# Performance work log

Measured on AMD Instinct MI355X. Metric: run time of the kernel, lower is better.

Reference implementation:

```python
import jax, jax.numpy as jnp
import numpy as np

N = 50000      # nodes
E = 800000     # edges (before self-loops)
IN_C = 128
HID = 32
HEADS = 4
OUT_C = 64
NEG_SLOPE = 0.2


def setup_inputs() -> dict:
    key = jax.random.key(0)
    ks = jax.random.split(key, 10)
    x = jax.random.normal(ks[0], (N, IN_C), dtype=jnp.float32)
    edge_index = jax.random.randint(ks[1], (2, E), 0, N, dtype=jnp.int32)
    # layer 1 params (GATConv(in_c, hid_c, heads=4), concat=True)
    W1 = jax.random.normal(ks[2], (IN_C, HEADS * HID), dtype=jnp.float32) / np.sqrt(IN_C)
    a_src1 = jax.random.normal(ks[3], (HEADS, HID), dtype=jnp.float32) / np.sqrt(HID)
    a_dst1 = jax.random.normal(ks[4], (HEADS, HID), dtype=jnp.float32) / np.sqrt(HID)
    b1 = jnp.zeros((HEADS * HID,), dtype=jnp.float32)
    # layer 2 params (GATConv(hid_c*heads, out_c, heads=1))
    W2 = jax.random.normal(ks[5], (HEADS * HID, OUT_C), dtype=jnp.float32) / np.sqrt(HEADS * HID)
    a_src2 = jax.random.normal(ks[6], (1, OUT_C), dtype=jnp.float32) / np.sqrt(OUT_C)
    a_dst2 = jax.random.normal(ks[7], (1, OUT_C), dtype=jnp.float32) / np.sqrt(OUT_C)
    b2 = jnp.zeros((OUT_C,), dtype=jnp.float32)
    return {"x": x, "edge_index": edge_index, "W1": W1, "a_src1": a_src1,
            "a_dst1": a_dst1, "b1": b1, "W2": W2, "a_src2": a_src2,
            "a_dst2": a_dst2, "b2": b2}


def _gat_layer(x, src, dst, self_mask, W, a_s, a_d, b, n):
    """One PyG-style GATConv: concat heads, leaky_relu(0.2), scatter-softmax over dst."""
    H, F = a_s.shape
    h = (x @ W).reshape(n, H, F)                       # [N, H, F]
    al_s = jnp.einsum('nhf,hf->nh', h, a_s)            # [N, H]
    al_d = jnp.einsum('nhf,hf->nh', h, a_d)
    e = al_s[src] + al_d[dst]                          # [E', H]
    e = jnp.where(e >= 0, e, NEG_SLOPE * e)            # leaky relu
    # emulate remove_self_loops on original edges (appended loops not masked)
    e = jnp.where(self_mask[:, None], -1e30, e)
    m = jax.ops.segment_max(e, dst, num_segments=n)    # per-dst max for stability
    p = jnp.exp(e - m[dst])
    p = jnp.where(self_mask[:, None], 0.0, p)
    denom = jax.ops.segment_sum(p, dst, num_segments=n) + 1e-16
    alpha = p / denom[dst]                             # [E', H]
    out = jax.ops.segment_sum(alpha[:, :, None] * h[src], dst, num_segments=n)
    return out.reshape(n, H * F) + b


def reference(x, edge_index, W1, a_src1, a_dst1, b1, W2, a_src2, a_dst2, b2):
    n = x.shape[0]
    src, dst = edge_index[0], edge_index[1]
    loops = jnp.arange(n, dtype=edge_index.dtype)
    src_a = jnp.concatenate([src, loops])
    dst_a = jnp.concatenate([dst, loops])
    # mask pre-existing self-loops (PyG removes then re-adds self loops)
    self_mask = jnp.concatenate([src == dst, jnp.zeros((n,), dtype=bool)])
    h = _gat_layer(x, src_a, dst_a, self_mask, W1, a_src1, a_dst1, b1, n)
    h = jax.nn.relu(h)
    return _gat_layer(h, src_a, dst_a, self_mask, W2, a_src2, a_dst2, b2, n)
```

## Files before the change

kernel.cpp:

```cpp
#include <hip/hip_runtime.h>

typedef unsigned short u16;
typedef unsigned int u32;
typedef __attribute__((ext_vector_type(8))) short bf16x8;
typedef __attribute__((ext_vector_type(4))) float f32x4;
typedef __attribute__((ext_vector_type(2))) float f32x2;

__device__ __forceinline__ float bf(u16 u){ return __uint_as_float(((u32)u) << 16); }
__device__ __forceinline__ float bf_lo(u32 u){ return __uint_as_float(u << 16); }
__device__ __forceinline__ float bf_hi(u32 u){ return __uint_as_float(u & 0xFFFF0000u); }
__device__ __forceinline__ u16 to_bf16(float f){
    u32 x = __float_as_uint(f);
    u32 r = (x + 0x7FFFu + ((x >> 16) & 1u)) >> 16;
    return (u16)r;
}
__device__ __forceinline__ float leaky(float v){ return (v >= 0.f) ? v : 0.2f * v; }
__device__ __forceinline__ float eexp(float v){
    return __expf(fminf(leaky(v), 80.f));
}
__device__ __forceinline__ f32x2 unpk2(u32 u){
    return (f32x2){bf_lo(u), bf_hi(u)};
}
__device__ __forceinline__ float ldany(const void* p, int i, int fl){
    return fl ? bf(((const u16*)p)[i]) : ((const float*)p)[i];
}
__device__ __forceinline__ u16 ldany_bf(const void* p, int i, int fl){
    return fl ? ((const u16*)p)[i] : to_bf16(((const float*)p)[i]);
}

constexpr int NS = 256;

struct HistCvtArgs {
    const int* dst; const int* src; int E; int chE; u16* cnt; int NBIN;
    const void* xin; u16* Xb; int nx;
    const void* W1; const void* W2; u16* W1t; u16* W2t;
    const void* vin[6]; float* vout[6];
    int* flag;
};
__global__ __launch_bounds__(256) void hist_cvt(HistCvtArgs a){
    int b = blockIdx.x;
    if (b < NS){
        __shared__ u32 hist[128];
        if (threadIdx.x < 128) hist[threadIdx.x] = 0;
        __syncthreads();
        int s0 = b * a.chE, s1 = min(a.E, s0 + a.chE);
        for (int i = s0 + threadIdx.x; i < s1; i += 256){
            int d = a.dst[i];
            if (a.src[i] != d) atomicAdd(&hist[d >> 9], 1);
        }
        __syncthreads();
        if (threadIdx.x < a.NBIN)
            a.cnt[threadIdx.x * NS + b] = (u16)hist[threadIdx.x];
        return;
    }
    __shared__ int sflag;
    const u16* x16 = (const u16*)a.xin;
    if (threadIdx.x < 64){
        int ok = 1;
        for (int i = threadIdx.x; i < 256; i += 64){
            u16 v = x16[i];
            int e = (v >> 7) & 0xFF;
            if (!((e >= 100 && e <= 140) || (v & 0x7FFFu) == 0)) ok = 0;
        }
        unsigned long long bl = __ballot(ok);
        if (threadIdx.x == 0) sflag = (__popcll(bl) >= 62) ? 1 : 0;
    }
    __syncthreads();
    int fl = sflag;
    int ci = (b - NS) * 256 + threadIdx.x;
    if (ci == 0) *a.flag = fl;
    if (ci < a.nx){ a.Xb[ci] = ldany_bf(a.xin, ci, fl); return; }
    ci -= a.nx;
    if (ci < 128 * 128){
        int n = ci >> 7, k = ci & 127;
        a.W1t[ci] = ldany_bf(a.W1, k * 128 + n, fl);
        return;
    }
    ci -= 128 * 128;
    if (ci < 64 * 128){
        int n = ci >> 7, k = ci & 127;
        a.W2t[ci] = ldany_bf(a.W2, k * 64 + n, fl);
        return;
    }
    ci -= 64 * 128;
    const int vsz[6] = {128, 128, 128, 64, 64, 64};
    #pragma unroll
    for (int s = 0; s < 6; s++){
        if (ci < vsz[s]){ a.vout[s][ci] = ldany(a.vin[s], ci, fl); return; }
        ci -= vsz[s];
    }
}

struct BucketGemmArgs {
    const int* dst; const int* src; int E; int chE; const u16* cnt; int NBIN;
    u32* Sbin;
    u32* bucket;
    const u16* Xb; const u16* W1t; u16* HB;
    const float* a_s; const float* a_d; float* al_s; float* al_d;
    int N;
};
__global__ __launch_bounds__(256) void bucket_gemm(BucketGemmArgs a){
    int b = blockIdx.x;
    if (b < NS){
        __shared__ u32 cur[128];
        __shared__ u32 Tl[129];
        int t = threadIdx.x;
        if (t < a.NBIN){
            const u16* row = a.cnt + (size_t)t * NS;
            u32 cb = 0, tot = 0;
            for (int sx = 0; sx < NS; sx++){
                u32 v = row[sx];
                tot += v;
                cb += (sx < b) ? v : 0u;
            }
            Tl[t + 1] = tot;
            cur[t] = cb;
        }
        __syncthreads();
        if (t == 0){
            u32 run = 0;
            Tl[0] = 0;
            for (int g = 1; g <= a.NBIN; g++){ run += Tl[g]; Tl[g] = run; }
        }
        __syncthreads();
        if (t < a.NBIN) cur[t] += Tl[t];
        if (b == 0 && t <= a.NBIN) a.Sbin[t] = Tl[t];
        __syncthreads();
        int s0 = b * a.chE, s1 = min(a.E, s0 + a.chE);
        for (int i = s0 + t; i < s1; i += 256){
            int d = a.dst[i];
            int s = a.src[i];
            if (s != d){
                u32 pos = atomicAdd(&cur[d >> 9], 1);
                a.bucket[pos] = ((u32)d << 16) | (u32)s;
            }
        }
        return;
    }
    int gb = b - NS;
    int lane = threadIdx.x & 63;
    int w = threadIdx.x >> 6;
    int row0 = gb * 64 + w * 16;
    int m = lane & 15, quad = lane >> 4;
    int arow = row0 + m;
    if (arow >= a.N) arow = a.N - 1;
    f32x4 acc[8];
    #pragma unroll
    for (int j = 0; j < 8; j++) acc[j] = (f32x4){0.f, 0.f, 0.f, 0.f};
    const u16* ap = a.Xb + (size_t)arow * 128 + quad * 8;
    const u16* bp = a.W1t + (size_t)m * 128 + quad * 8;
    #pragma unroll
    for (int kc = 0; kc < 4; kc++){
        bf16x8 av = *(const bf16x8*)(ap + kc * 32);
        #pragma unroll
        for (int nb = 0; nb < 8; nb++){
            bf16x8 bv = *(const bf16x8*)(bp + nb * 16 * 128 + kc * 32);
            acc[nb] = __builtin_amdgcn_mfma_f32_16x16x32_bf16(av, bv, acc[nb], 0, 0, 0);
        }
    }
    #pragma unroll
    for (int nb = 0; nb < 8; nb++){
        #pragma unroll
        for (int r = 0; r < 4; r++){
            int grow = row0 + quad * 4 + r;
            if (grow < a.N) a.HB[(size_t)grow * 128 + nb * 16 + m] = to_bf16(acc[nb][r]);
        }
    }
    float asr[8], adr[8];
    #pragma unroll
    for (int nb = 0; nb < 8; nb++){ asr[nb] = a.a_s[nb * 16 + m]; adr[nb] = a.a_d[nb * 16 + m]; }
    #pragma unroll
    for (int r = 0; r < 4; r++){
        int grow = row0 + quad * 4 + r;
        #pragma unroll
        for (int h = 0; h < 4; h++){
            float ps = acc[2 * h][r] * asr[2 * h] + acc[2 * h + 1][r] * asr[2 * h + 1];
            float pd = acc[2 * h][r] * adr[2 * h] + acc[2 * h + 1][r] * adr[2 * h + 1];
            #pragma unroll
            for (int d = 1; d < 16; d <<= 1){
                ps += __shfl_xor(ps, d);
                pd += __shfl_xor(pd, d);
            }
            if (m == h && grow < a.N){
                a.al_s[grow * 4 + h] = ps;
                a.al_d[grow * 4 + h] = pd;
            }
        }
    }
}

__global__ __launch_bounds__(256) void bin_csr(const u32* __restrict__ Sbin,
                                               const u32* __restrict__ bucket,
                                               int* __restrict__ off,
                                               u16* __restrict__ csr,
                                               int N, int NBIN){
    __shared__ u32 degL[512];
    __shared__ u32 curL[512];
    __shared__ int wsum[4];
    int b = blockIdx.x, t = threadIdx.x;
    int lo = b << 9;
    u32 base = Sbin[b];
    u32 end  = Sbin[b + 1];
    degL[t] = 0; degL[t + 256] = 0;
    __syncthreads();
    for (u32 i = base + t; i < end; i += 256){
        u32 pr = bucket[i];
        atomicAdd(&degL[(pr >> 16) - lo], 1);
    }
    __syncthreads();
    u32 d0 = degL[2 * t], d1 = degL[2 * t + 1];
    int p = (int)(d0 + d1);
    int v = p;
    #pragma unroll
    for (int d = 1; d < 64; d <<= 1){
        int o = __shfl_up(v, d);
        if ((t & 63) >= d) v += o;
    }
    if ((t & 63) == 63) wsum[t >> 6] = v;
    __syncthreads();
    int woff = 0;
    for (int wv = 0; wv < (t >> 6); wv++) woff += wsum[wv];
    int eb = woff + v - p;
    curL[2 * t] = eb;
    curL[2 * t + 1] = eb + d0;
    int n0 = lo + 2 * t, n1 = lo + 2 * t + 1;
    if (n0 < N) off[n0] = (int)(base + eb);
    if (n1 < N) off[n1] = (int)(base + eb + d0);
    if (b == NBIN - 1 && t == 255) off[N] = (int)end;
    __syncthreads();
    for (u32 i = base + t; i < end; i += 256){
        u32 pr = bucket[i];
        u32 pos = base + atomicAdd(&curL[(pr >> 16) - lo], 1);
        csr[pos] = (u16)(pr & 0xFFFF);
    }
}

__global__ __launch_bounds__(256) void gemm2_logits(const u16* __restrict__ Xb,
                                                    const u16* __restrict__ Wt,
                                                    u16* __restrict__ HB,
                                                    const float* __restrict__ a_s,
                                                    const float* __restrict__ a_d,
                                                    float* __restrict__ al_s,
                                                    float* __restrict__ al_d, int N){
    int lane = threadIdx.x & 63;
    int w = threadIdx.x >> 6;
    int row0 = blockIdx.x * 64 + w * 16;
    int m = lane & 15, quad = lane >> 4;
    int arow = row0 + m;
    if (arow >= N) arow = N - 1;
    f32x4 acc[4];
    #pragma unroll
    for (int j = 0; j < 4; j++) acc[j] = (f32x4){0.f, 0.f, 0.f, 0.f};
    const u16* ap = Xb + (size_t)arow * 128 + quad * 8;
    const u16* bp = Wt + (size_t)m * 128 + quad * 8;
    #pragma unroll
    for (int kc = 0; kc < 4; kc++){
        bf16x8 av = *(const bf16x8*)(ap + kc * 32);
        #pragma unroll
        for (int nb = 0; nb < 4; nb++){
            bf16x8 bv = *(const bf16x8*)(bp + nb * 16 * 128 + kc * 32);
            acc[nb] = __builtin_amdgcn_mfma_f32_16x16x32_bf16(av, bv, acc[nb], 0, 0, 0);
        }
    }
    #pragma unroll
    for (int nb = 0; nb < 4; nb++){
        #pragma unroll
        for (int r = 0; r < 4; r++){
            int grow = row0 + quad * 4 + r;
            if (grow < N) HB[(size_t)grow * 64 + nb * 16 + m] = to_bf16(acc[nb][r]);
        }
    }
    float asr[4], adr[4];
    #pragma unroll
    for (int nb = 0; nb < 4; nb++){ asr[nb] = a_s[nb * 16 + m]; adr[nb] = a_d[nb * 16 + m]; }
    #pragma unroll
    for (int r = 0; r < 4; r++){
        int grow = row0 + quad * 4 + r;
        float ps = 0.f, pd = 0.f;
        #pragma unroll
        for (int nb = 0; nb < 4; nb++){ ps += acc[nb][r] * asr[nb]; pd += acc[nb][r] * adr[nb]; }
        #pragma unroll
        for (int d = 1; d < 16; d <<= 1){
            ps += __shfl_xor(ps, d);
            pd += __shfl_xor(pd, d);
        }
        if (m == 0 && grow < N){
            al_s[grow] = ps;
            al_d[grow] = pd;
        }
    }
}

__global__ __launch_bounds__(256) void gat_agg1(const int* __restrict__ off,
                                                const u16* __restrict__ csr,
                                                const u16* __restrict__ h1,
                                                const float* __restrict__ als,
                                                const float* __restrict__ ald,
                                                const float* __restrict__ b1,
                                                u16* __restrict__ outm, int N){
    int lane = threadIdx.x & 63;
    int n = blockIdx.x * 4 + (threadIdx.x >> 6);
    if (n >= N) return;
    int o0 = off[n], o1 = off[n + 1];
    int q = lane >> 4, ql = lane & 15;
    int c0 = ql * 8;
    int head = ql >> 2;
    float aldh = ald[n * 4 + head];
    f32x2 a0 = {0.f, 0.f}, a1 = {0.f, 0.f}, a2 = {0.f, 0.f}, a3 = {0.f, 0.f};
    float s = 0.f;
    int j = o0 + q;
    for (; j + 12 < o1; j += 16){
        int sc0 = csr[j], sc1 = csr[j + 4], sc2 = csr[j + 8], sc3 = csr[j + 12];
        float e0 = eexp(als[sc0 * 4 + head] + aldh);
        float e1 = eexp(als[sc1 * 4 + head] + aldh);
        float e2 = eexp(als[sc2 * 4 + head] + aldh);
        float e3 = eexp(als[sc3 * 4 + head] + aldh);
        uint4 u0 = *(const uint4*)&h1[(size_t)sc0 * 128 + c0];
        uint4 u1 = *(const uint4*)&h1[(size_t)sc1 * 128 + c0];
        uint4 u2 = *(const uint4*)&h1[(size_t)sc2 * 128 + c0];
        uint4 u3 = *(const uint4*)&h1[(size_t)sc3 * 128 + c0];
        s += (e0 + e1) + (e2 + e3);
        f32x2 ev0 = {e0, e0}, ev1 = {e1, e1}, ev2 = {e2, e2}, ev3 = {e3, e3};
        a0 += ev0 * unpk2(u0.x); a1 += ev0 * unpk2(u0.y);
        a2 += ev0 * unpk2(u0.z); a3 += ev0 * unpk2(u0.w);
        a0 += ev1 * unpk2(u1.x); a1 += ev1 * unpk2(u1.y);
        a2 += ev1 * unpk2(u1.z); a3 += ev1 * unpk2(u1.w);
        a0 += ev2 * unpk2(u2.x); a1 += ev2 * unpk2(u2.y);
        a2 += ev2 * unpk2(u2.z); a3 += ev2 * unpk2(u2.w);
        a0 += ev3 * unpk2(u3.x); a1 += ev3 * unpk2(u3.y);
        a2 += ev3 * unpk2(u3.z); a3 += ev3 * unpk2(u3.w);
    }
    for (; j < o1; j += 4){
        int sc = csr[j];
        float e = eexp(als[sc * 4 + head] + aldh);
        uint4 u = *(const uint4*)&h1[(size_t)sc * 128 + c0];
        s += e;
        f32x2 ev = {e, e};
        a0 += ev * unpk2(u.x); a1 += ev * unpk2(u.y);
        a2 += ev * unpk2(u.z); a3 += ev * unpk2(u.w);
    }
    float acc[8] = {a0.x, a0.y, a1.x, a1.y, a2.x, a2.y, a3.x, a3.y};
    s += __shfl_xor(s, 16);
    s += __shfl_xor(s, 32);
    #pragma unroll
    for (int i = 0; i < 8; i++){
        acc[i] += __shfl_xor(acc[i], 16);
        acc[i] += __shfl_xor(acc[i], 32);
    }
    if (q == 0){
        float esx = eexp(als[n * 4 + head] + aldh);
        float inv = 1.f / (s + esx + 1e-16f);
        uint4 u = *(const uint4*)&h1[(size_t)n * 128 + c0];
        acc[0] += esx * bf_lo(u.x); acc[1] += esx * bf_hi(u.x);
        acc[2] += esx * bf_lo(u.y); acc[3] += esx * bf_hi(u.y);
        acc[4] += esx * bf_lo(u.z); acc[5] += esx * bf_hi(u.z);
        acc[6] += esx * bf_lo(u.w); acc[7] += esx * bf_hi(u.w);
        float4 bA = *(const float4*)&b1[c0];
        float4 bB = *(const float4*)&b1[c0 + 4];
        u16 pk[8];
        pk[0] = to_bf16(fmaxf(acc[0] * inv + bA.x, 0.f));
        pk[1] = to_bf16(fmaxf(acc[1] * inv + bA.y, 0.f));
        pk[2] = to_bf16(fmaxf(acc[2] * inv + bA.z, 0.f));
        pk[3] = to_bf16(fmaxf(acc[3] * inv + bA.w, 0.f));
        pk[4] = to_bf16(fmaxf(acc[4] * inv + bB.x, 0.f));
        pk[5] = to_bf16(fmaxf(acc[5] * inv + bB.y, 0.f));
        pk[6] = to_bf16(fmaxf(acc[6] * inv + bB.z, 0.f));
        pk[7] = to_bf16(fmaxf(acc[7] * inv + bB.w, 0.f));
        *(uint4*)&outm[(size_t)n * 128 + c0] = *(uint4*)pk;
    }
}

__global__ __launch_bounds__(256) void gat_agg2(const int* __restrict__ off,
                                                const u16* __restrict__ csr,
                                                const u16* __restrict__ h2,
                                                const float* __restrict__ als,
                                                const float* __restrict__ ald,
                                                const float* __restrict__ b2,
                                                void* __restrict__ outv, int N,
                                                const int* __restrict__ flag){
    int lane = threadIdx.x & 63;
    int n = blockIdx.x * 4 + (threadIdx.x >> 6);
    if (n >= N) return;
    int o0 = off[n], o1 = off[n + 1];
    int oc = lane >> 3, ol = lane & 7;
    int c0 = ol * 8;
    float aldn = ald[n];
    f32x2 a0 = {0.f, 0.f}, a1 = {0.f, 0.f}, a2 = {0.f, 0.f}, a3 = {0.f, 0.f};
    float s = 0.f;
    int j = o0 + oc;
    for (; j + 8 < o1; j += 16){
        int sc0 = csr[j], sc1 = csr[j + 8];
        float e0 = eexp(als[sc0] + aldn);
        float e1 = eexp(als[sc1] + aldn);
        uint4 u0 = *(const uint4*)&h2[(size_t)sc0 * 64 + c0];
        uint4 u1 = *(const uint4*)&h2[(size_t)sc1 * 64 + c0];
        s += e0 + e1;
        f32x2 ev0 = {e0, e0}, ev1 = {e1, e1};
        a0 += ev0 * unpk2(u0.x); a1 += ev0 * unpk2(u0.y);
        a2 += ev0 * unpk2(u0.z); a3 += ev0 * unpk2(u0.w);
        a0 += ev1 * unpk2(u1.x); a1 += ev1 * unpk2(u1.y);
        a2 += ev1 * unpk2(u1.z); a3 += ev1 * unpk2(u1.w);
    }
    if (j < o1){
        int sc = csr[j];
        float e = eexp(als[sc] + aldn);
        uint4 u = *(const uint4*)&h2[(size_t)sc * 64 + c0];
        s += e;
        f32x2 ev = {e, e};
        a0 += ev * unpk2(u.x); a1 += ev * unpk2(u.y);
        a2 += ev * unpk2(u.z); a3 += ev * unpk2(u.w);
    }
    float acc[8] = {a0.x, a0.y, a1.x, a1.y, a2.x, a2.y, a3.x, a3.y};
    s += __shfl_xor(s, 8);
    s += __shfl_xor(s, 16);
    s += __shfl_xor(s, 32);
    #pragma unroll
    for (int i = 0; i < 8; i++){
        acc[i] += __shfl_xor(acc[i], 8);
        acc[i] += __shfl_xor(acc[i], 16);
        acc[i] += __shfl_xor(acc[i], 32);
    }
    if (oc == 0){
        float esx = eexp(als[n] + aldn);
        float inv = 1.f / (s + esx + 1e-16f);
        uint4 u = *(const uint4*)&h2[(size_t)n * 64 + c0];
        acc[0] += esx * bf_lo(u.x); acc[1] += esx * bf_hi(u.x);
        acc[2] += esx * bf_lo(u.y); acc[3] += esx * bf_hi(u.y);
        acc[4] += esx * bf_lo(u.z); acc[5] += esx * bf_hi(u.z);
        acc[6] += esx * bf_lo(u.w); acc[7] += esx * bf_hi(u.w);
        float4 bA = *(const float4*)&b2[c0];
        float4 bB = *(const float4*)&b2[c0 + 4];
        float r[8];
        r[0] = acc[0] * inv + bA.x; r[1] = acc[1] * inv + bA.y;
        r[2] = acc[2] * inv + bA.z; r[3] = acc[3] * inv + bA.w;
        r[4] = acc[4] * inv + bB.x; r[5] = acc[5] * inv + bB.y;
        r[6] = acc[6] * inv + bB.z; r[7] = acc[7] * inv + bB.w;
        if (*flag){
            u16 pk[8];
            #pragma unroll
            for (int i = 0; i < 8; i++) pk[i] = to_bf16(r[i]);
            *(uint4*)&((u16*)outv)[(size_t)n * 64 + c0] = *(uint4*)pk;
        } else {
            float* op = &((float*)outv)[(size_t)n * 64 + c0];
            *(float4*)op = make_float4(r[0], r[1], r[2], r[3]);
            *(float4*)(op + 4) = make_float4(r[4], r[5], r[6], r[7]);
        }
    }
}

extern "C" void kernel_launch(void* const* d_in, const int* in_sizes, int n_in,
                              void* d_out, int out_size, void* d_ws, size_t ws_size,
                              hipStream_t stream){
    const int* ei  = (const int*)d_in[1];
    const int N = in_sizes[0] / 128;
    const int E = in_sizes[1] / 2;
    const int* src = ei;
    const int* dst = ei + E;
    const int NBIN = (N + 511) >> 9;
    const int chE  = (E + NS - 1) / NS;

    char* w = (char*)d_ws;
    auto alloc = [&](size_t bytes){ char* p = w; w += (bytes + 255) & ~(size_t)255; return p; };
    int*   flag  = (int*)  alloc(4);
    u16*   cnt   = (u16*)  alloc((size_t)NS * NBIN * 2);
    u32*   Sbin  = (u32*)  alloc((size_t)(NBIN + 1) * 4);
    u32*   bucket= (u32*)  alloc((size_t)E * 4);
    int*   off   = (int*)  alloc((size_t)(N + 1) * 4);
    u16*   csr   = (u16*)  alloc((size_t)E * 2);
    u16*   W1t   = (u16*)  alloc(128 * 128 * 2);
    u16*   W2t   = (u16*)  alloc(64 * 128 * 2);
    float* as1f  = (float*)alloc(128 * 4);
    float* ad1f  = (float*)alloc(128 * 4);
    float* b1f   = (float*)alloc(128 * 4);
    float* as2f  = (float*)alloc(64 * 4);
    float* ad2f  = (float*)alloc(64 * 4);
    float* b2f   = (float*)alloc(64 * 4);
    u16*   Xb    = (u16*)  alloc((size_t)N * 128 * 2);
    u16*   h1b   = (u16*)  alloc((size_t)N * 128 * 2);
    u16*   hmidb = (u16*)  alloc((size_t)N * 128 * 2);
    u16*   h2b   = (u16*)  alloc((size_t)N * 64 * 2);
    float* als1  = (float*)alloc((size_t)N * 4 * 4);
    float* ald1  = (float*)alloc((size_t)N * 4 * 4);
    float* als2  = als1;
    float* ald2  = ald1;

    HistCvtArgs k1;
    k1.dst = dst; k1.src = src; k1.E = E; k1.chE = chE; k1.cnt = cnt; k1.NBIN = NBIN;
    k1.xin = d_in[0]; k1.Xb = Xb; k1.nx = N * 128;
    k1.W1 = d_in[2]; k1.W2 = d_in[6]; k1.W1t = W1t; k1.W2t = W2t;
    const void* vin[6]  = {d_in[3], d_in[4], d_in[5], d_in[7], d_in[8], d_in[9]};
    float* vout[6] = {as1f, ad1f, b1f, as2f, ad2f, b2f};
    for (int s = 0; s < 6; s++){ k1.vin[s] = vin[s]; k1.vout[s] = vout[s]; }
    k1.flag = flag;
    int cvt_total = N * 128 + 128 * 128 + 64 * 128 + 576;
    hist_cvt<<<NS + (cvt_total + 255) / 256, 256, 0, stream>>>(k1);

    BucketGemmArgs k3;
    k3.dst = dst; k3.src = src; k3.E = E; k3.chE = chE; k3.cnt = cnt; k3.NBIN = NBIN;
    k3.Sbin = Sbin;
    k3.bucket = bucket;
    k3.Xb = Xb; k3.W1t = W1t; k3.HB = h1b;
    k3.a_s = as1f; k3.a_d = ad1f; k3.al_s = als1; k3.al_d = ald1;
    k3.N = N;
    bucket_gemm<<<NS + (N + 63) / 64, 256, 0, stream>>>(k3);

    bin_csr<<<NBIN, 256, 0, stream>>>(Sbin, bucket, off, csr, N, NBIN);

    gat_agg1<<<(N + 3) / 4, 256, 0, stream>>>(off, csr, h1b, als1, ald1, b1f, hmidb, N);

    gemm2_logits<<<(N + 63) / 64, 256, 0, stream>>>(hmidb, W2t, h2b, as2f, ad2f, als2, ald2, N);

    gat_agg2<<<(N + 3) / 4, 256, 0, stream>>>(off, csr, h2b, als2, ald2, b2f, d_out, N, flag);
}
```

Baseline: 229.5 us.

## Fuse layer-1 aggregation with layer-2 GEMM and logits via shared memory

Merges the layer-1 neighbor aggregation kernel and the layer-2 MFMA GEMM/logit kernel into one kernel. Each block aggregates 16 nodes (each wave handles 4 sequentially) into a shared-memory tile, then one wave runs the 16x64 GEMM and attention-logit reductions. This drops the global write and reread of the hidden activations and one kernel launch. In exchange, each wave now processes nodes serially, and three of the four waves idle during the GEMM phase, which may reduce memory-level parallelism in the gather.

```diff
diff --git a/kernel.cpp b/kernel.cpp
--- a/kernel.cpp
+++ b/kernel.cpp
@@ -235,138 +235,142 @@
     }
 }
 
-__global__ __launch_bounds__(256) void gemm2_logits(const u16* __restrict__ Xb,
-                                                    const u16* __restrict__ Wt,
-                                                    u16* __restrict__ HB,
-                                                    const float* __restrict__ a_s,
-                                                    const float* __restrict__ a_d,
-                                                    float* __restrict__ al_s,
-                                                    float* __restrict__ al_d, int N){
+__global__ __launch_bounds__(256) void agg1_gemm2(const int* __restrict__ off,
+                                                  const u16* __restrict__ csr,
+                                                  const u16* __restrict__ h1,
+                                                  const float* __restrict__ als,
+                                                  const float* __restrict__ ald,
+                                                  const float* __restrict__ b1,
+                                                  const u16* __restrict__ W2t,
+                                                  const float* __restrict__ as2,
+                                                  const float* __restrict__ ad2,
+                                                  u16* __restrict__ h2b,
+                                                  float* __restrict__ als2,
+                                                  float* __restrict__ ald2,
+                                                  int N){
+    __shared__ u16 hm[16][136];
     int lane = threadIdx.x & 63;
     int w = threadIdx.x >> 6;
-    int row0 = blockIdx.x * 64 + w * 16;
+    int base = blockIdx.x * 16;
+    int q = lane >> 4, ql = lane & 15;
+    int c0 = ql * 8;
+    int head = ql >> 2;
+    #pragma unroll 1
+    for (int it = 0; it < 4; it++){
+        int row = w * 4 + it;
+        int n = base + row;
+        if (n < N){
+            int o0 = off[n], o1 = off[n + 1];
+            float aldh = ald[n * 4 + head];
+            f32x2 a0 = {0.f, 0.f}, a1 = {0.f, 0.f}, a2 = {0.f, 0.f}, a3 = {0.f, 0.f};
+            float s = 0.f;
+            int j = o0 + q;
+            for (; j + 12 < o1; j += 16){
+                int sc0 = csr[j], sc1 = csr[j + 4], sc2 = csr[j + 8], sc3 = csr[j + 12];
+                float e0 = eexp(als[sc0 * 4 + head] + aldh);
+                float e1 = eexp(als[sc1 * 4 + head] + aldh);
+                float e2 = eexp(als[sc2 * 4 + head] + aldh);
+                float e3 = eexp(als[sc3 * 4 + head] + aldh);
+                uint4 u0 = *(const uint4*)&h1[(size_t)sc0 * 128 + c0];
+                uint4 u1 = *(const uint4*)&h1[(size_t)sc1 * 128 + c0];
+                uint4 u2 = *(const uint4*)&h1[(size_t)sc2 * 128 + c0];
+                uint4 u3 = *(const uint4*)&h1[(size_t)sc3 * 128 + c0];
+                s += (e0 + e1) + (e2 + e3);
+                f32x2 ev0 = {e0, e0}, ev1 = {e1, e1}, ev2 = {e2, e2}, ev3 = {e3, e3};
+                a0 += ev0 * unpk2(u0.x); a1 += ev0 * unpk2(u0.y);
+                a2 += ev0 * unpk2(u0.z); a3 += ev0 * unpk2(u0.w);
+                a0 += ev1 * unpk2(u1.x); a1 += ev1 * unpk2(u1.y);
+                a2 += ev1 * unpk2(u1.z); a3 += ev1 * unpk2(u1.w);
+                a0 += ev2 * unpk2(u2.x); a1 += ev2 * unpk2(u2.y);
+                a2 += ev2 * unpk2(u2.z); a3 += ev2 * unpk2(u2.w);
+                a0 += ev3 * unpk2(u3.x); a1 += ev3 * unpk2(u3.y);
+                a2 += ev3 * unpk2(u3.z); a3 += ev3 * unpk2(u3.w);
+            }
+            for (; j < o1; j += 4){
+                int sc = csr[j];
+                float e = eexp(als[sc * 4 + head] + aldh);
+                uint4 u = *(const uint4*)&h1[(size_t)sc * 128 + c0];
+                s += e;
+                f32x2 ev = {e, e};
+                a0 += ev * unpk2(u.x); a1 += ev * unpk2(u.y);
+                a2 += ev * unpk2(u.z); a3 += ev * unpk2(u.w);
+            }
+            float acc[8] = {a0.x, a0.y, a1.x, a1.y, a2.x, a2.y, a3.x, a3.y};
+            s += __shfl_xor(s, 16);
+            s += __shfl_xor(s, 32);
+            #pragma unroll
+            for (int i = 0; i < 8; i++){
+                acc[i] += __shfl_xor(acc[i], 16);
+                acc[i] += __shfl_xor(acc[i], 32);
+            }
+            if (q == 0){
+                float esx = eexp(als[n * 4 + head] + aldh);
+                float inv = 1.f / (s + esx + 1e-16f);
+                uint4 u = *(const uint4*)&h1[(size_t)n * 128 + c0];
+                acc[0] += esx * bf_lo(u.x); acc[1] += esx * bf_hi(u.x);
+                acc[2] += esx * bf_lo(u.y); acc[3] += esx * bf_hi(u.y);
+                acc[4] += esx * bf_lo(u.z); acc[5] += esx * bf_hi(u.z);
+                acc[6] += esx * bf_lo(u.w); acc[7] += esx * bf_hi(u.w);
+                float4 bA = *(const float4*)&b1[c0];
+                float4 bB = *(const float4*)&b1[c0 + 4];
+                u16 pk[8];
+                pk[0] = to_bf16(fmaxf(acc[0] * inv + bA.x, 0.f));
+                pk[1] = to_bf16(fmaxf(acc[1] * inv + bA.y, 0.f));
+                pk[2] = to_bf16(fmaxf(acc[2] * inv + bA.z, 0.f));
+                pk[3] = to_bf16(fmaxf(acc[3] * inv + bA.w, 0.f));
+                pk[4] = to_bf16(fmaxf(acc[4] * inv + bB.x, 0.f));
+                pk[5] = to_bf16(fmaxf(acc[5] * inv + bB.y, 0.f));
+                pk[6] = to_bf16(fmaxf(acc[6] * inv + bB.z, 0.f));
+                pk[7] = to_bf16(fmaxf(acc[7] * inv + bB.w, 0.f));
+                *(uint4*)&hm[row][c0] = *(uint4*)pk;
+            }
+        } else if (q == 0){
+            *(uint4*)&hm[row][c0] = make_uint4(0, 0, 0, 0);
+        }
+    }
+    __syncthreads();
+    if (w != 0) return;
     int m = lane & 15, quad = lane >> 4;
-    int arow = row0 + m;
-    if (arow >= N) arow = N - 1;
-    f32x4 acc[4];
-    #pragma unroll
-    for (int j = 0; j < 4; j++) acc[j] = (f32x4){0.f, 0.f, 0.f, 0.f};
-    const u16* ap = Xb + (size_t)arow * 128 + quad * 8;
-    const u16* bp = Wt + (size_t)m * 128 + quad * 8;
+    f32x4 acc2[4];
+    #pragma unroll
+    for (int j = 0; j < 4; j++) acc2[j] = (f32x4){0.f, 0.f, 0.f, 0.f};
+    const u16* ap = &hm[m][quad * 8];
+    const u16* bp = W2t + (size_t)m * 128 + quad * 8;
     #pragma unroll
     for (int kc = 0; kc < 4; kc++){
         bf16x8 av = *(const bf16x8*)(ap + kc * 32);
         #pragma unroll
         for (int nb = 0; nb < 4; nb++){
             bf16x8 bv = *(const bf16x8*)(bp + nb * 16 * 128 + kc * 32);
-            acc[nb] = __builtin_amdgcn_mfma_f32_16x16x32_bf16(av, bv, acc[nb], 0, 0, 0);
+            acc2[nb] = __builtin_amdgcn_mfma_f32_16x16x32_bf16(av, bv, acc2[nb], 0, 0, 0);
         }
     }
     #pragma unroll
     for (int nb = 0; nb < 4; nb++){
         #pragma unroll
         for (int r = 0; r < 4; r++){
-            int grow = row0 + quad * 4 + r;
-            if (grow < N) HB[(size_t)grow * 64 + nb * 16 + m] = to_bf16(acc[nb][r]);
+            int grow = base + quad * 4 + r;
+            if (grow < N) h2b[(size_t)grow * 64 + nb * 16 + m] = to_bf16(acc2[nb][r]);
         }
     }
     float asr[4], adr[4];
     #pragma unroll
-    for (int nb = 0; nb < 4; nb++){ asr[nb] = a_s[nb * 16 + m]; adr[nb] = a_d[nb * 16 + m]; }
+    for (int nb = 0; nb < 4; nb++){ asr[nb] = as2[nb * 16 + m]; adr[nb] = ad2[nb * 16 + m]; }
     #pragma unroll
     for (int r = 0; r < 4; r++){
-        int grow = row0 + quad * 4 + r;
+        int grow = base + quad * 4 + r;
         float ps = 0.f, pd = 0.f;
         #pragma unroll
-        for (int nb = 0; nb < 4; nb++){ ps += acc[nb][r] * asr[nb]; pd += acc[nb][r] * adr[nb]; }
+        for (int nb = 0; nb < 4; nb++){ ps += acc2[nb][r] * asr[nb]; pd += acc2[nb][r] * adr[nb]; }
         #pragma unroll
         for (int d = 1; d < 16; d <<= 1){
             ps += __shfl_xor(ps, d);
             pd += __shfl_xor(pd, d);
         }
         if (m == 0 && grow < N){
-            al_s[grow] = ps;
-            al_d[grow] = pd;
-        }
-    }
-}
-
-__global__ __launch_bounds__(256) void gat_agg1(const int* __restrict__ off,
-                                                const u16* __restrict__ csr,
-                                                const u16* __restrict__ h1,
-                                                const float* __restrict__ als,
-                                                const float* __restrict__ ald,
-                                                const float* __restrict__ b1,
-                                                u16* __restrict__ outm, int N){
-    int lane = threadIdx.x & 63;
-    int n = blockIdx.x * 4 + (threadIdx.x >> 6);
-    if (n >= N) return;
-    int o0 = off[n], o1 = off[n + 1];
-    int q = lane >> 4, ql = lane & 15;
-    int c0 = ql * 8;
-    int head = ql >> 2;
-    float aldh = ald[n * 4 + head];
-    f32x2 a0 = {0.f, 0.f}, a1 = {0.f, 0.f}, a2 = {0.f, 0.f}, a3 = {0.f, 0.f};
-    float s = 0.f;
-    int j = o0 + q;
-    for (; j + 12 < o1; j += 16){
-        int sc0 = csr[j], sc1 = csr[j + 4], sc2 = csr[j + 8], sc3 = csr[j + 12];
-        float e0 = eexp(als[sc0 * 4 + head] + aldh);
-        float e1 = eexp(als[sc1 * 4 + head] + aldh);
-        float e2 = eexp(als[sc2 * 4 + head] + aldh);
-        float e3 = eexp(als[sc3 * 4 + head] + aldh);
-        uint4 u0 = *(const uint4*)&h1[(size_t)sc0 * 128 + c0];
-        uint4 u1 = *(const uint4*)&h1[(size_t)sc1 * 128 + c0];
-        uint4 u2 = *(const uint4*)&h1[(size_t)sc2 * 128 + c0];
-        uint4 u3 = *(const uint4*)&h1[(size_t)sc3 * 128 + c0];
-        s += (e0 + e1) + (e2 + e3);
-        f32x2 ev0 = {e0, e0}, ev1 = {e1, e1}, ev2 = {e2, e2}, ev3 = {e3, e3};
-        a0 += ev0 * unpk2(u0.x); a1 += ev0 * unpk2(u0.y);
-        a2 += ev0 * unpk2(u0.z); a3 += ev0 * unpk2(u0.w);
-        a0 += ev1 * unpk2(u1.x); a1 += ev1 * unpk2(u1.y);
-        a2 += ev1 * unpk2(u1.z); a3 += ev1 * unpk2(u1.w);
-        a0 += ev2 * unpk2(u2.x); a1 += ev2 * unpk2(u2.y);
-        a2 += ev2 * unpk2(u2.z); a3 += ev2 * unpk2(u2.w);
-        a0 += ev3 * unpk2(u3.x); a1 += ev3 * unpk2(u3.y);
-        a2 += ev3 * unpk2(u3.z); a3 += ev3 * unpk2(u3.w);
-    }
-    for (; j < o1; j += 4){
-        int sc = csr[j];
-        float e = eexp(als[sc * 4 + head] + aldh);
-        uint4 u = *(const uint4*)&h1[(size_t)sc * 128 + c0];
-        s += e;
-        f32x2 ev = {e, e};
-        a0 += ev * unpk2(u.x); a1 += ev * unpk2(u.y);
-        a2 += ev * unpk2(u.z); a3 += ev * unpk2(u.w);
-    }
-    float acc[8] = {a0.x, a0.y, a1.x, a1.y, a2.x, a2.y, a3.x, a3.y};
-    s += __shfl_xor(s, 16);
-    s += __shfl_xor(s, 32);
-    #pragma unroll
-    for (int i = 0; i < 8; i++){
-        acc[i] += __shfl_xor(acc[i], 16);
-        acc[i] += __shfl_xor(acc[i], 32);
-    }
-    if (q == 0){
-        float esx = eexp(als[n * 4 + head] + aldh);
-        float inv = 1.f / (s + esx + 1e-16f);
-        uint4 u = *(const uint4*)&h1[(size_t)n * 128 + c0];
-        acc[0] += esx * bf_lo(u.x); acc[1] += esx * bf_hi(u.x);
-        acc[2] += esx * bf_lo(u.y); acc[3] += esx * bf_hi(u.y);
-        acc[4] += esx * bf_lo(u.z); acc[5] += esx * bf_hi(u.z);
-        acc[6] += esx * bf_lo(u.w); acc[7] += esx * bf_hi(u.w);
-        float4 bA = *(const float4*)&b1[c0];
-        float4 bB = *(const float4*)&b1[c0 + 4];
-        u16 pk[8];
-        pk[0] = to_bf16(fmaxf(acc[0] * inv + bA.x, 0.f));
-        pk[1] = to_bf16(fmaxf(acc[1] * inv + bA.y, 0.f));
-        pk[2] = to_bf16(fmaxf(acc[2] * inv + bA.z, 0.f));
-        pk[3] = to_bf16(fmaxf(acc[3] * inv + bA.w, 0.f));
-        pk[4] = to_bf16(fmaxf(acc[4] * inv + bB.x, 0.f));
-        pk[5] = to_bf16(fmaxf(acc[5] * inv + bB.y, 0.f));
-        pk[6] = to_bf16(fmaxf(acc[6] * inv + bB.z, 0.f));
-        pk[7] = to_bf16(fmaxf(acc[7] * inv + bB.w, 0.f));
-        *(uint4*)&outm[(size_t)n * 128 + c0] = *(uint4*)pk;
+            als2[grow] = ps;
+            ald2[grow] = pd;
+        }
     }
 }
 
@@ -477,12 +481,11 @@
     float* b2f   = (float*)alloc(64 * 4);
     u16*   Xb    = (u16*)  alloc((size_t)N * 128 * 2);
     u16*   h1b   = (u16*)  alloc((size_t)N * 128 * 2);
-    u16*   hmidb = (u16*)  alloc((size_t)N * 128 * 2);
     u16*   h2b   = (u16*)  alloc((size_t)N * 64 * 2);
     float* als1  = (float*)alloc((size_t)N * 4 * 4);
     float* ald1  = (float*)alloc((size_t)N * 4 * 4);
-    float* als2  = als1;
-    float* ald2  = ald1;
+    float* als2  = (float*)alloc((size_t)N * 4);
+    float* ald2  = (float*)alloc((size_t)N * 4);
 
     HistCvtArgs k1;
     k1.dst = dst; k1.src = src; k1.E = E; k1.chE = chE; k1.cnt = cnt; k1.NBIN = NBIN;
@@ -506,9 +509,8 @@
 
     bin_csr<<<NBIN, 256, 0, stream>>>(Sbin, bucket, off, csr, N, NBIN);
 
-    gat_agg1<<<(N + 3) / 4, 256, 0, stream>>>(off, csr, h1b, als1, ald1, b1f, hmidb, N);
-
-    gemm2_logits<<<(N + 63) / 64, 256, 0, stream>>>(hmidb, W2t, h2b, as2f, ad2f, als2, ald2, N);
+    agg1_gemm2<<<(N + 15) / 16, 256, 0, stream>>>(off, csr, h1b, als1, ald1, b1f,
+                                                  W2t, as2f, ad2f, h2b, als2, ald2, N);
 
     gat_agg2<<<(N + 3) / 4, 256, 0, stream>>>(off, csr, h2b, als2, ald2, b2f, d_out, N, flag);
 }
```

New measurement: 242.0 us. +5.4%, slower.
